# Performance work log

Measured on AMD Instinct MI355X. Metric: run time of the kernel, lower is better.

## Reference

```python
import jax, jax.numpy as jnp
import numpy as np

EMBED_DIM = 768
NUM_HEADS = 12
HEAD_DIM = EMBED_DIM // NUM_HEADS
SCALING = HEAD_DIM ** -0.5
B, S = 2, 2048


def setup_inputs() -> dict:
    key = jax.random.key(0)
    k1, k2, k3 = jax.random.split(key, 3)
    x_q = jax.random.normal(k1, (B, S, EMBED_DIM), dtype=jnp.float32)
    # xavier-uniform-ish scaling for weights
    lim_qkv = (6.0 / (EMBED_DIM + 3 * EMBED_DIM)) ** 0.5
    lim_out = (6.0 / (2 * EMBED_DIM)) ** 0.5
    w_qkv = jax.random.uniform(k2, (3 * EMBED_DIM, EMBED_DIM), jnp.float32, -lim_qkv, lim_qkv)
    b_qkv = jnp.zeros((3 * EMBED_DIM,), jnp.float32)
    w_out = jax.random.uniform(k3, (EMBED_DIM, EMBED_DIM), jnp.float32, -lim_out, lim_out)
    b_out = jnp.zeros((EMBED_DIM,), jnp.float32)
    return {"x_q": x_q, "w_qkv": w_qkv, "b_qkv": b_qkv, "w_out": w_out, "b_out": b_out}


def reference(x_q, w_qkv, b_qkv, w_out, b_out):
    b_sz, s_len, _ = x_q.shape
    # qkv projection: (B,S,3E) -> (B,S,3,H,hd) -> split
    qkv = x_q @ w_qkv.T + b_qkv
    qkv = qkv.reshape(b_sz, s_len, 3, NUM_HEADS, HEAD_DIM)
    q = qkv[:, :, 0].transpose(0, 2, 1, 3) * SCALING  # (B,H,S,hd)
    k = qkv[:, :, 1].transpose(0, 2, 1, 3)
    v = qkv[:, :, 2].transpose(0, 2, 1, 3)
    attn = jnp.einsum("bhsd,bhtd->bhst", q, k)  # (B,H,S,S)
    attn = jax.nn.softmax(attn.astype(jnp.float32), axis=-1).astype(attn.dtype)
    out = jnp.einsum("bhst,bhtd->bhsd", attn, v)  # (B,H,S,hd)
    out = out.transpose(0, 2, 1, 3).reshape(b_sz, s_len, EMBED_DIM)
    return out @ w_out.T + b_out
```

## Files before the change

kernel.cpp:

```cpp
#include <hip/hip_runtime.h>
#include <hip/hip_bf16.h>
#include <math.h>

typedef unsigned short u16;
typedef unsigned int u32;
typedef __attribute__((ext_vector_type(8))) short bf16x8;
typedef __attribute__((ext_vector_type(4))) short bf16x4;
typedef __attribute__((ext_vector_type(4))) float f32x4;

#define EMBED 768
#define NHEADS 12
#define HDIM 64
#define NBATCH 2
#define SEQ 2048
#define NTOK 4096
#define QKV_N 2304
#define BHTOT 24
#define QSCALE 0.18033688011112042f

__device__ __forceinline__ u16 f2b(float f) {
    __hip_bfloat16 h = __float2bfloat16(f);
    return __builtin_bit_cast(u16, h);
}
__device__ __forceinline__ u32 pk2(float a, float b) {
    return (u32)f2b(a) | ((u32)f2b(b) << 16);
}
__device__ __forceinline__ f32x4 mfma32(bf16x8 a, bf16x8 b, f32x4 c) {
    return __builtin_amdgcn_mfma_f32_16x16x32_bf16(a, b, c, 0, 0, 0);
}
#if __has_builtin(__builtin_amdgcn_mfma_f32_16x16x16_bf16)
__device__ __forceinline__ f32x4 mfma16(bf16x4 a, bf16x4 b, f32x4 c) {
    return __builtin_amdgcn_mfma_f32_16x16x16_bf16(a, b, c, 0, 0, 0);
}
#else
__device__ __forceinline__ f32x4 mfma16(bf16x4 a, bf16x4 b, f32x4 c) {
    return __builtin_amdgcn_mfma_f32_16x16x16bf16_1k(a, b, c, 0, 0, 0);
}
#endif

__device__ __forceinline__ float exp2_hw(float x) {
#if __has_builtin(__builtin_amdgcn_exp2f)
    return __builtin_amdgcn_exp2f(x);
#else
    float r;
    asm("v_exp_f32 %0, %1" : "=v"(r) : "v"(x));
    return r;
#endif
}

__device__ __forceinline__ void async16(const u16* g, u16* l) {
    __builtin_amdgcn_global_load_lds(
        (const __attribute__((address_space(1))) unsigned int*)g,
        (__attribute__((address_space(3))) unsigned int*)l,
        16, 0, 0);
}

__global__ __launch_bounds__(256)
void cast_kernel(const float* __restrict__ s0, u16* __restrict__ d0, int n0,
                 const float* __restrict__ s1, u16* __restrict__ d1, int n1,
                 const float* __restrict__ s2, u16* __restrict__ d2, int n2)
{
    int idx = (blockIdx.x * 256 + threadIdx.x) * 4;
    const float* s; u16* d; int i;
    if (idx < n0)            { s = s0; d = d0; i = idx; }
    else if (idx < n0 + n1)  { s = s1; d = d1; i = idx - n0; }
    else                     { s = s2; d = d2; i = idx - n0 - n1; if (i >= n2) return; }
    float4 v = *(const float4*)&s[i];
    ushort4 o;
    o.x = f2b(v.x); o.y = f2b(v.y); o.z = f2b(v.z); o.w = f2b(v.w);
    *(ushort4*)&d[i] = o;
}

__global__ __launch_bounds__(256)
void qkv_gemm(const u16* __restrict__ A, const u16* __restrict__ W,
              const float* __restrict__ bias,
              u16* __restrict__ Qb, u16* __restrict__ Kb, u16* __restrict__ VT)
{
    __shared__ __align__(16) u16 smem[4 * 8192];
    u16* As = smem;
    u16* Bs = smem + 2 * 8192;
    const int m0 = blockIdx.x * 128;
    const int n0 = blockIdx.y * 128;
    const int tid = threadIdx.x;
    const int w = tid >> 6, l = tid & 63;
    const int c = l & 15, q = l >> 4;
    const int wm = (w >> 1) * 64, wn = (w & 1) * 64;
    const int r8 = l >> 3, ch = l & 7;
    const int gch = ch ^ r8;

    #pragma unroll
    for (int j = 0; j < 4; ++j) {
        int row = w * 32 + j * 8 + r8;
        int seg = (w * 32 + j * 8) * 64;
        async16(&A[(size_t)(m0 + row) * EMBED + gch * 8], &As[seg + l * 8]);
        async16(&W[(size_t)(n0 + row) * EMBED + gch * 8], &Bs[seg + l * 8]);
    }

    f32x4 acc[4][4] = {};
    const int NK = EMBED / 64;

    #pragma unroll 2
    for (int kt = 0; kt < NK; ++kt) {
        const int cur = kt & 1;
        __syncthreads();
        if (kt + 1 < NK) {
            int k0 = (kt + 1) * 64;
            #pragma unroll
            for (int j = 0; j < 4; ++j) {
                int row = w * 32 + j * 8 + r8;
                int seg = (cur ^ 1) * 8192 + (w * 32 + j * 8) * 64;
                async16(&A[(size_t)(m0 + row) * EMBED + k0 + gch * 8], &As[seg + l * 8]);
                async16(&W[(size_t)(n0 + row) * EMBED + k0 + gch * 8], &Bs[seg + l * 8]);
            }
        }
        const u16* Ab = As + cur * 8192;
        const u16* Bb = Bs + cur * 8192;
        #pragma unroll
        for (int ks = 0; ks < 2; ++ks) {
            const int cs = (((ks << 2) | q) ^ (c & 7)) << 3;
            bf16x8 af[4], bfr[4];
            #pragma unroll
            for (int i = 0; i < 4; ++i)
                af[i] = *(const bf16x8*)&Ab[(wm + i * 16 + c) * 64 + cs];
            #pragma unroll
            for (int j = 0; j < 4; ++j)
                bfr[j] = *(const bf16x8*)&Bb[(wn + j * 16 + c) * 64 + cs];
            #pragma unroll
            for (int i = 0; i < 4; ++i)
                #pragma unroll
                for (int j = 0; j < 4; ++j)
                    acc[i][j] = mfma32(af[i], bfr[j], acc[i][j]);
        }
    }

    const int p = n0 / EMBED;
    const int ncol0 = n0 + wn;
    const int h = (ncol0 % EMBED) / HDIM;
    const int mrow0 = m0 + wm;
    const int b = mrow0 >> 11;
    const int s0 = mrow0 & (SEQ - 1);

    if (p < 2) {
        u16* dst = (p == 0) ? Qb : Kb;
        const float mul = (p == 0) ? QSCALE : 1.0f;
        #pragma unroll
        for (int j = 0; j < 4; ++j) {
            int n = ncol0 + j * 16 + c;
            int d = j * 16 + c;
            float bval = bias[n];
            #pragma unroll
            for (int i = 0; i < 4; ++i) {
                #pragma unroll
                for (int r = 0; r < 4; ++r) {
                    int s = s0 + i * 16 + q * 4 + r;
                    float v = (acc[i][j][r] + bval) * mul;
                    dst[(((size_t)(b * NHEADS + h)) * SEQ + s) * HDIM + d] = f2b(v);
                }
            }
        }
    } else {
        __syncthreads();
        u16* T = smem + w * (64 * 72);
        #pragma unroll
        for (int j = 0; j < 4; ++j) {
            int n = ncol0 + j * 16 + c;
            float bval = bias[n];
            #pragma unroll
            for (int i = 0; i < 4; ++i) {
                uint2 pr;
                pr.x = pk2(acc[i][j][0] + bval, acc[i][j][1] + bval);
                pr.y = pk2(acc[i][j][2] + bval, acc[i][j][3] + bval);
                *(uint2*)&T[(j * 16 + c) * 72 + i * 16 + q * 4] = pr;
            }
        }
        const size_t vtbase = ((size_t)(b * NHEADS + h)) * HDIM * SEQ + s0;
        #pragma unroll
        for (int ii = 0; ii < 8; ++ii) {
            int d = (l >> 3) + 8 * ii;
            int sch = (l & 7) * 8;
            uint4 vv = *(const uint4*)&T[d * 72 + sch];
            *(uint4*)&VT[vtbase + (size_t)d * SEQ + sch] = vv;
        }
    }
}

__global__ __launch_bounds__(256, 3)
void attn_kernel(const u16* __restrict__ Qb, const u16* __restrict__ Kb,
                 const u16* __restrict__ VT, u16* __restrict__ AO)
{
    __shared__ __align__(16) u16 Ks[3][4096];
    __shared__ __align__(16) u16 Vs[3][4096];

    const int blk = blockIdx.x;
    const int g = blk & 7, kk = blk >> 3;
    const int bh = g * 3 + (kk >> 5);
    const int qt = kk & 31;

    const int tid = threadIdx.x;
    const int w = tid >> 6, l = tid & 63;
    const int c = l & 15, q = l >> 4;
    const int wq = w >> 1, wk = w & 1;

    const u16* qg = Qb + ((size_t)bh * SEQ + qt * 64 + wq * 32) * HDIM;
    const u16* kg = Kb + ((size_t)bh * SEQ) * HDIM;
    const u16* vg = VT + ((size_t)bh * HDIM) * SEQ;

    const int r8 = l >> 3, ch = l & 7;
    const int gch = ch ^ r8;

    bf16x8 bq[2][2];
    #pragma unroll
    for (int qb2 = 0; qb2 < 2; ++qb2) {
        bq[qb2][0] = *(const bf16x8*)&qg[(qb2 * 16 + c) * HDIM + q * 8];
        bq[qb2][1] = *(const bf16x8*)&qg[(qb2 * 16 + c) * HDIM + 32 + q * 8];
    }

    f32x4 o[4][2] = {};
    float lrow[2] = {0.f, 0.f};

    const int NT = SEQ / 64;

#define STAGE(JT, BS) {                                                       \
    int row0 = w * 16 + r8;                                                   \
    async16(&kg[(size_t)((JT) * 64 + row0) * HDIM + gch * 8],                 \
            &Ks[BS][(w * 16) * 64 + l * 8]);                                  \
    async16(&vg[(size_t)row0 * SEQ + (JT) * 64 + gch * 8],                    \
            &Vs[BS][(w * 16) * 64 + l * 8]);                                  \
    async16(&kg[(size_t)((JT) * 64 + row0 + 8) * HDIM + gch * 8],             \
            &Ks[BS][(w * 16 + 8) * 64 + l * 8]);                              \
    async16(&vg[(size_t)(row0 + 8) * SEQ + (JT) * 64 + gch * 8],              \
            &Vs[BS][(w * 16 + 8) * 64 + l * 8]);                              \
}

#define QKT(SN, BN) {                                                         \
    __builtin_amdgcn_s_setprio(1);                                            \
    _Pragma("unroll")                                                         \
    for (int kb2 = 0; kb2 < 2; ++kb2) {                                       \
        bf16x8 ak0 = *(const bf16x8*)&Ks[BN][(wk * 32 + kb2 * 16 + c) * 64 +  \
                                             (((q    ) ^ (c & 7)) << 3)];     \
        bf16x8 ak1 = *(const bf16x8*)&Ks[BN][(wk * 32 + kb2 * 16 + c) * 64 +  \
                                             (((q | 4) ^ (c & 7)) << 3)];     \
        _Pragma("unroll")                                                     \
        for (int qb2 = 0; qb2 < 2; ++qb2) {                                   \
            f32x4 zz = {};                                                    \
            zz = mfma32(ak0, bq[qb2][0], zz);                                 \
            SN[kb2][qb2] = mfma32(ak1, bq[qb2][1], zz);                       \
        }                                                                     \
    }                                                                         \
    __builtin_amdgcn_s_setprio(0);                                            \
}

#define SOFTPV(SC, BC) {                                                      \
    _Pragma("unroll")                                                         \
    for (int kb2 = 0; kb2 < 2; ++kb2)                                         \
        _Pragma("unroll")                                                     \
        for (int qb2 = 0; qb2 < 2; ++qb2) {                                   \
            float p0 = exp2_hw(SC[kb2][qb2][0]);                              \
            float p1 = exp2_hw(SC[kb2][qb2][1]);                              \
            float p2 = exp2_hw(SC[kb2][qb2][2]);                              \
            float p3 = exp2_hw(SC[kb2][qb2][3]);                              \
            SC[kb2][qb2][0] = p0; SC[kb2][qb2][1] = p1;                       \
            SC[kb2][qb2][2] = p2; SC[kb2][qb2][3] = p3;                       \
            lrow[qb2] += (p0 + p1) + (p2 + p3);                               \
        }                                                                     \
    bf16x4 bp[2][2];                                                          \
    _Pragma("unroll")                                                         \
    for (int kb2 = 0; kb2 < 2; ++kb2)                                         \
        _Pragma("unroll")                                                     \
        for (int qb2 = 0; qb2 < 2; ++qb2) {                                   \
            uint2 pr;                                                         \
            pr.x = pk2(SC[kb2][qb2][0], SC[kb2][qb2][1]);                     \
            pr.y = pk2(SC[kb2][qb2][2], SC[kb2][qb2][3]);                     \
            bp[kb2][qb2] = __builtin_bit_cast(bf16x4, pr);                    \
        }                                                                     \
    __builtin_amdgcn_s_setprio(1);                                            \
    _Pragma("unroll")                                                         \
    for (int db = 0; db < 4; ++db) {                                          \
        bf16x4 av0 = *(const bf16x4*)&Vs[BC][(db * 16 + c) * 64 +             \
                  (((4 * wk     + (q >> 1)) ^ (c & 7)) << 3) + ((q & 1) << 2)]; \
        bf16x4 av1 = *(const bf16x4*)&Vs[BC][(db * 16 + c) * 64 +             \
                  (((4 * wk + 2 + (q >> 1)) ^ (c & 7)) << 3) + ((q & 1) << 2)]; \
        _Pragma("unroll")                                                     \
        for (int qb2 = 0; qb2 < 2; ++qb2) {                                   \
            o[db][qb2] = mfma16(av0, bp[0][qb2], o[db][qb2]);                 \
            o[db][qb2] = mfma16(av1, bp[1][qb2], o[db][qb2]);                 \
        }                                                                     \
    }                                                                         \
    __builtin_amdgcn_s_setprio(0);                                            \
}

#define BODY(J, SC, SN, BC, BN, BS) {                                         \
    asm volatile("s_waitcnt vmcnt(0)" ::: "memory");                          \
    __builtin_amdgcn_s_barrier();                                             \
    if ((J) + 2 < NT) STAGE((J) + 2, BS);                                     \
    if ((J) + 1 < NT) QKT(SN, BN);                                            \
    SOFTPV(SC, BC);                                                           \
}

    f32x4 scA[2][2], scB[2][2];

    STAGE(0, 0);
    STAGE(1, 1);
    asm volatile("s_waitcnt vmcnt(4)" ::: "memory");
    __builtin_amdgcn_s_barrier();
    QKT(scA, 0);

    for (int jb = 0; jb < 30; jb += 6) {
        BODY(jb + 0, scA, scB, 0, 1, 2);
        BODY(jb + 1, scB, scA, 1, 2, 0);
        BODY(jb + 2, scA, scB, 2, 0, 1);
        BODY(jb + 3, scB, scA, 0, 1, 2);
        BODY(jb + 4, scA, scB, 1, 2, 0);
        BODY(jb + 5, scB, scA, 2, 0, 1);
    }
    BODY(30, scA, scB, 0, 1, 2);
    SOFTPV(scB, 1);

#undef STAGE
#undef QKT
#undef SOFTPV
#undef BODY

    #pragma unroll
    for (int qb2 = 0; qb2 < 2; ++qb2) {
        lrow[qb2] += __shfl_xor(lrow[qb2], 16);
        lrow[qb2] += __shfl_xor(lrow[qb2], 32);
    }

    __syncthreads();
    float* SCR = (float*)&Ks[0][0];
    float* LR  = SCR + 4096;

    if (wk == 1) {
        #pragma unroll
        for (int db = 0; db < 4; ++db)
            #pragma unroll
            for (int qb2 = 0; qb2 < 2; ++qb2)
                *(f32x4*)&SCR[((wq * 8 + db * 2 + qb2) << 8) + l * 4] = o[db][qb2];
        if (q == 0) {
            LR[(wq * 2 + 0) * 16 + c] = lrow[0];
            LR[(wq * 2 + 1) * 16 + c] = lrow[1];
        }
    }
    __syncthreads();

    if (wk == 0) {
        float inv[2];
        #pragma unroll
        for (int qb2 = 0; qb2 < 2; ++qb2)
            inv[qb2] = 1.0f / (lrow[qb2] + LR[(wq * 2 + qb2) * 16 + c]);
        const int b = bh / NHEADS, h = bh % NHEADS;
        #pragma unroll
        for (int qb2 = 0; qb2 < 2; ++qb2) {
            const int s = qt * 64 + wq * 32 + qb2 * 16 + c;
            u16* ao = AO + ((size_t)(b * SEQ + s)) * EMBED + h * HDIM;
            #pragma unroll
            for (int db = 0; db < 4; ++db) {
                f32x4 part = *(const f32x4*)&SCR[((wq * 8 + db * 2 + qb2) << 8) + l * 4];
                f32x4 t = o[db][qb2] + part;
                uint2 oo;
                oo.x = pk2(t[0] * inv[qb2], t[1] * inv[qb2]);
                oo.y = pk2(t[2] * inv[qb2], t[3] * inv[qb2]);
                *(uint2*)&ao[db * 16 + q * 4] = oo;
            }
        }
    }
}

__global__ __launch_bounds__(256)
void out_gemm(const u16* __restrict__ A, const u16* __restrict__ W,
              const float* __restrict__ bias, float* __restrict__ out)
{
    __shared__ __align__(16) u16 As[2][8192];
    __shared__ __align__(16) u16 Bs[2][4096];
    const int m0 = blockIdx.x * 128;
    const int n0 = blockIdx.y * 64;
    const int tid = threadIdx.x;
    const int w = tid >> 6, l = tid & 63;
    const int c = l & 15, q = l >> 4;
    const int wm = w * 32;
    const int r8 = l >> 3, ch = l & 7;
    const int gch = ch ^ r8;

    #pragma unroll
    for (int j = 0; j < 4; ++j) {
        int row = w * 32 + j * 8 + r8;
        async16(&A[(size_t)(m0 + row) * EMBED + gch * 8],
                &As[0][(w * 32 + j * 8) * 64 + l * 8]);
    }
    #pragma unroll
    for (int j = 0; j < 2; ++j) {
        int row = w * 16 + j * 8 + r8;
        async16(&W[(size_t)(n0 + row) * EMBED + gch * 8],
                &Bs[0][(w * 16 + j * 8) * 64 + l * 8]);
    }

    f32x4 acc[2][4] = {};
    const int NK = EMBED / 64;

    #pragma unroll 2
    for (int kt = 0; kt < NK; ++kt) {
        const int cur = kt & 1;
        __syncthreads();
        if (kt + 1 < NK) {
            int k0 = (kt + 1) * 64;
            #pragma unroll
            for (int j = 0; j < 4; ++j) {
                int row = w * 32 + j * 8 + r8;
                async16(&A[(size_t)(m0 + row) * EMBED + k0 + gch * 8],
                        &As[cur ^ 1][(w * 32 + j * 8) * 64 + l * 8]);
            }
            #pragma unroll
            for (int j = 0; j < 2; ++j) {
                int row = w * 16 + j * 8 + r8;
                async16(&W[(size_t)(n0 + row) * EMBED + k0 + gch * 8],
                        &Bs[cur ^ 1][(w * 16 + j * 8) * 64 + l * 8]);
            }
        }
        #pragma unroll
        for (int ks = 0; ks < 2; ++ks) {
            const int cs = (((ks << 2) | q) ^ (c & 7)) << 3;
            bf16x8 af[2], bfr[4];
            #pragma unroll
            for (int i = 0; i < 2; ++i)
                af[i] = *(const bf16x8*)&As[cur][(wm + i * 16 + c) * 64 + cs];
            #pragma unroll
            for (int j = 0; j < 4; ++j)
                bfr[j] = *(const bf16x8*)&Bs[cur][(j * 16 + c) * 64 + cs];
            #pragma unroll
            for (int i = 0; i < 2; ++i)
                #pragma unroll
                for (int j = 0; j < 4; ++j)
                    acc[i][j] = mfma32(af[i], bfr[j], acc[i][j]);
        }
    }

    #pragma unroll
    for (int j = 0; j < 4; ++j) {
        int n = n0 + j * 16 + c;
        float bval = bias[n];
        #pragma unroll
        for (int i = 0; i < 2; ++i) {
            #pragma unroll
            for (int r = 0; r < 4; ++r) {
                int m = m0 + wm + i * 16 + q * 4 + r;
                out[(size_t)m * EMBED + n] = acc[i][j][r] + bval;
            }
        }
    }
}

extern "C" void kernel_launch(void* const* d_in, const int* in_sizes, int n_in,
                              void* d_out, int out_size, void* d_ws, size_t ws_size,
                              hipStream_t stream)
{
    const float* x    = (const float*)d_in[0];
    const float* wqkv = (const float*)d_in[1];
    const float* bqkv = (const float*)d_in[2];
    const float* wout = (const float*)d_in[3];
    const float* bout = (const float*)d_in[4];
    float* out = (float*)d_out;

    const int nx  = NTOK * EMBED;
    const int nwq = QKV_N * EMBED;
    const int nwo = EMBED * EMBED;
    const size_t per = (size_t)NBATCH * NHEADS * SEQ * HDIM;

    u16* xb    = (u16*)d_ws;
    u16* wqkvb = xb + nx;
    u16* woutb = wqkvb + nwq;
    u16* Qb    = woutb + nwo;
    u16* Kb    = Qb + per;
    u16* VT    = Kb + per;
    u16* AO    = VT + per;

    int castTot = (nx + nwq + nwo) / 4;
    cast_kernel<<<castTot / 256, 256, 0, stream>>>(x, xb, nx, wqkv, wqkvb, nwq, wout, woutb, nwo);

    dim3 g1(NTOK / 128, QKV_N / 128);
    qkv_gemm<<<g1, 256, 0, stream>>>(xb, wqkvb, bqkv, Qb, Kb, VT);

    attn_kernel<<<BHTOT * 32, 256, 0, stream>>>(Qb, Kb, VT, AO);

    dim3 g3(NTOK / 128, EMBED / 64);
    out_gemm<<<g3, 256, 0, stream>>>(AO, woutb, bout, out);
}
```

Measured before the change: 149.9 us.

## Shrink K-tile to 32 in QKV GEMM and use smaller out-GEMM tiles

The QKV GEMM drops its K-step from 64 to 32, which cuts shared memory per block so several blocks can reside per CU. It also adds a launch-bounds occupancy hint and a matching XOR swizzle for the narrower rows. The output GEMM moves from 128x64 to 64x64 tiles with a 32-wide K-step, doubling its grid to fill more CUs. The cost is twice as many barriers and loop iterations and less data reuse per loaded tile.

```diff
diff --git a/kernel.cpp b/kernel.cpp
--- a/kernel.cpp
+++ b/kernel.cpp
@@ -71,66 +71,63 @@
     *(ushort4*)&d[i] = o;
 }
 
-__global__ __launch_bounds__(256)
+__global__ __launch_bounds__(256, 4)
 void qkv_gemm(const u16* __restrict__ A, const u16* __restrict__ W,
               const float* __restrict__ bias,
               u16* __restrict__ Qb, u16* __restrict__ Kb, u16* __restrict__ VT)
 {
-    __shared__ __align__(16) u16 smem[4 * 8192];
+    __shared__ __align__(16) u16 smem[18432];
     u16* As = smem;
-    u16* Bs = smem + 2 * 8192;
+    u16* Bs = smem + 8192;
     const int m0 = blockIdx.x * 128;
     const int n0 = blockIdx.y * 128;
     const int tid = threadIdx.x;
     const int w = tid >> 6, l = tid & 63;
     const int c = l & 15, q = l >> 4;
     const int wm = (w >> 1) * 64, wn = (w & 1) * 64;
-    const int r8 = l >> 3, ch = l & 7;
-    const int gch = ch ^ r8;
+    const int sr = l >> 2;
+    const int gch2 = (l & 3) ^ ((l >> 3) & 3);
 
     #pragma unroll
-    for (int j = 0; j < 4; ++j) {
-        int row = w * 32 + j * 8 + r8;
-        int seg = (w * 32 + j * 8) * 64;
-        async16(&A[(size_t)(m0 + row) * EMBED + gch * 8], &As[seg + l * 8]);
-        async16(&W[(size_t)(n0 + row) * EMBED + gch * 8], &Bs[seg + l * 8]);
+    for (int j = 0; j < 2; ++j) {
+        int row = j * 64 + w * 16 + sr;
+        int seg = (j * 64 + w * 16) * 32;
+        async16(&A[(size_t)(m0 + row) * EMBED + gch2 * 8], &As[seg + l * 8]);
+        async16(&W[(size_t)(n0 + row) * EMBED + gch2 * 8], &Bs[seg + l * 8]);
     }
 
     f32x4 acc[4][4] = {};
-    const int NK = EMBED / 64;
+    const int NK = EMBED / 32;
 
     #pragma unroll 2
     for (int kt = 0; kt < NK; ++kt) {
         const int cur = kt & 1;
         __syncthreads();
         if (kt + 1 < NK) {
-            int k0 = (kt + 1) * 64;
-            #pragma unroll
-            for (int j = 0; j < 4; ++j) {
-                int row = w * 32 + j * 8 + r8;
-                int seg = (cur ^ 1) * 8192 + (w * 32 + j * 8) * 64;
-                async16(&A[(size_t)(m0 + row) * EMBED + k0 + gch * 8], &As[seg + l * 8]);
-                async16(&W[(size_t)(n0 + row) * EMBED + k0 + gch * 8], &Bs[seg + l * 8]);
+            int k0 = (kt + 1) * 32;
+            #pragma unroll
+            for (int j = 0; j < 2; ++j) {
+                int row = j * 64 + w * 16 + sr;
+                int seg = (cur ^ 1) * 4096 + (j * 64 + w * 16) * 32;
+                async16(&A[(size_t)(m0 + row) * EMBED + k0 + gch2 * 8], &As[seg + l * 8]);
+                async16(&W[(size_t)(n0 + row) * EMBED + k0 + gch2 * 8], &Bs[seg + l * 8]);
             }
         }
-        const u16* Ab = As + cur * 8192;
-        const u16* Bb = Bs + cur * 8192;
-        #pragma unroll
-        for (int ks = 0; ks < 2; ++ks) {
-            const int cs = (((ks << 2) | q) ^ (c & 7)) << 3;
-            bf16x8 af[4], bfr[4];
-            #pragma unroll
-            for (int i = 0; i < 4; ++i)
-                af[i] = *(const bf16x8*)&Ab[(wm + i * 16 + c) * 64 + cs];
+        const u16* Ab = As + cur * 4096;
+        const u16* Bb = Bs + cur * 4096;
+        const int cs = (q ^ ((c >> 1) & 3)) << 3;
+        bf16x8 af[4], bfr[4];
+        #pragma unroll
+        for (int i = 0; i < 4; ++i)
+            af[i] = *(const bf16x8*)&Ab[(wm + i * 16 + c) * 32 + cs];
+        #pragma unroll
+        for (int j = 0; j < 4; ++j)
+            bfr[j] = *(const bf16x8*)&Bb[(wn + j * 16 + c) * 32 + cs];
+        #pragma unroll
+        for (int i = 0; i < 4; ++i)
             #pragma unroll
             for (int j = 0; j < 4; ++j)
-                bfr[j] = *(const bf16x8*)&Bb[(wn + j * 16 + c) * 64 + cs];
-            #pragma unroll
-            for (int i = 0; i < 4; ++i)
-                #pragma unroll
-                for (int j = 0; j < 4; ++j)
-                    acc[i][j] = mfma32(af[i], bfr[j], acc[i][j]);
-        }
+                acc[i][j] = mfma32(af[i], bfr[j], acc[i][j]);
     }
 
     const int p = n0 / EMBED;
@@ -371,68 +368,46 @@
 void out_gemm(const u16* __restrict__ A, const u16* __restrict__ W,
               const float* __restrict__ bias, float* __restrict__ out)
 {
-    __shared__ __align__(16) u16 As[2][8192];
-    __shared__ __align__(16) u16 Bs[2][4096];
-    const int m0 = blockIdx.x * 128;
+    __shared__ __align__(16) u16 As[2][2048];
+    __shared__ __align__(16) u16 Bs[2][2048];
+    const int m0 = blockIdx.x * 64;
     const int n0 = blockIdx.y * 64;
     const int tid = threadIdx.x;
     const int w = tid >> 6, l = tid & 63;
     const int c = l & 15, q = l >> 4;
-    const int wm = w * 32;
-    const int r8 = l >> 3, ch = l & 7;
-    const int gch = ch ^ r8;
-
-    #pragma unroll
-    for (int j = 0; j < 4; ++j) {
-        int row = w * 32 + j * 8 + r8;
-        async16(&A[(size_t)(m0 + row) * EMBED + gch * 8],
-                &As[0][(w * 32 + j * 8) * 64 + l * 8]);
-    }
-    #pragma unroll
-    for (int j = 0; j < 2; ++j) {
-        int row = w * 16 + j * 8 + r8;
-        async16(&W[(size_t)(n0 + row) * EMBED + gch * 8],
-                &Bs[0][(w * 16 + j * 8) * 64 + l * 8]);
-    }
-
-    f32x4 acc[2][4] = {};
-    const int NK = EMBED / 64;
+    const int sr = l >> 2;
+    const int gch2 = (l & 3) ^ ((l >> 3) & 3);
+
+    {
+        int row = w * 16 + sr;
+        async16(&A[(size_t)(m0 + row) * EMBED + gch2 * 8], &As[0][(w * 16) * 32 + l * 8]);
+        async16(&W[(size_t)(n0 + row) * EMBED + gch2 * 8], &Bs[0][(w * 16) * 32 + l * 8]);
+    }
+
+    f32x4 acc[4] = {};
+    const int NK = EMBED / 32;
 
     #pragma unroll 2
     for (int kt = 0; kt < NK; ++kt) {
         const int cur = kt & 1;
         __syncthreads();
         if (kt + 1 < NK) {
-            int k0 = (kt + 1) * 64;
-            #pragma unroll
-            for (int j = 0; j < 4; ++j) {
-                int row = w * 32 + j * 8 + r8;
-                async16(&A[(size_t)(m0 + row) * EMBED + k0 + gch * 8],
-                        &As[cur ^ 1][(w * 32 + j * 8) * 64 + l * 8]);
-            }
-            #pragma unroll
-            for (int j = 0; j < 2; ++j) {
-                int row = w * 16 + j * 8 + r8;
-                async16(&W[(size_t)(n0 + row) * EMBED + k0 + gch * 8],
-                        &Bs[cur ^ 1][(w * 16 + j * 8) * 64 + l * 8]);
-            }
-        }
-        #pragma unroll
-        for (int ks = 0; ks < 2; ++ks) {
-            const int cs = (((ks << 2) | q) ^ (c & 7)) << 3;
-            bf16x8 af[2], bfr[4];
-            #pragma unroll
-            for (int i = 0; i < 2; ++i)
-                af[i] = *(const bf16x8*)&As[cur][(wm + i * 16 + c) * 64 + cs];
-            #pragma unroll
-            for (int j = 0; j < 4; ++j)
-                bfr[j] = *(const bf16x8*)&Bs[cur][(j * 16 + c) * 64 + cs];
-            #pragma unroll
-            for (int i = 0; i < 2; ++i)
-                #pragma unroll
-                for (int j = 0; j < 4; ++j)
-                    acc[i][j] = mfma32(af[i], bfr[j], acc[i][j]);
-        }
+            int k0 = (kt + 1) * 32;
+            int row = w * 16 + sr;
+            async16(&A[(size_t)(m0 + row) * EMBED + k0 + gch2 * 8],
+                    &As[cur ^ 1][(w * 16) * 32 + l * 8]);
+            async16(&W[(size_t)(n0 + row) * EMBED + k0 + gch2 * 8],
+                    &Bs[cur ^ 1][(w * 16) * 32 + l * 8]);
+        }
+        const int cs = (q ^ ((c >> 1) & 3)) << 3;
+        bf16x8 af = *(const bf16x8*)&As[cur][(w * 16 + c) * 32 + cs];
+        bf16x8 bfr[4];
+        #pragma unroll
+        for (int j = 0; j < 4; ++j)
+            bfr[j] = *(const bf16x8*)&Bs[cur][(j * 16 + c) * 32 + cs];
+        #pragma unroll
+        for (int j = 0; j < 4; ++j)
+            acc[j] = mfma32(af, bfr[j], acc[j]);
     }
 
     #pragma unroll
@@ -440,12 +415,9 @@
         int n = n0 + j * 16 + c;
         float bval = bias[n];
         #pragma unroll
-        for (int i = 0; i < 2; ++i) {
-            #pragma unroll
-            for (int r = 0; r < 4; ++r) {
-                int m = m0 + wm + i * 16 + q * 4 + r;
-                out[(size_t)m * EMBED + n] = acc[i][j][r] + bval;
-            }
+        for (int r = 0; r < 4; ++r) {
+            int m = m0 + w * 16 + q * 4 + r;
+            out[(size_t)m * EMBED + n] = acc[j][r] + bval;
         }
     }
 }
@@ -482,6 +454,6 @@
 
     attn_kernel<<<BHTOT * 32, 256, 0, stream>>>(Qb, Kb, VT, AO);
 
-    dim3 g3(NTOK / 128, EMBED / 64);
+    dim3 g3(NTOK / 64, EMBED / 64);
     out_gemm<<<g3, 256, 0, stream>>>(AO, woutb, bout, out);
 }
```

After: 149.9 us (median of 2 runs). Within noise of the previous version (+0.0%).
